# Kernel optimization log

Measured on AMD Instinct MI355X. Metric: run time of the kernel, lower is better.

## Reference

```python
import jax, jax.numpy as jnp
import numpy as np

NUM_HEADS = 64  # init kwarg


def _split_heads(x, num_heads):
    # torch: x.view(N, num_heads, head_size).permute(0, 2, 1) -> [N, head_size, num_heads]
    n, hidden = x.shape
    head_size = hidden // num_heads
    return x.reshape(n, num_heads, head_size).transpose(0, 2, 1)


def setup_inputs() -> dict:
    key = jax.random.key(0)
    kq, kk, kv = jax.random.split(key, 3)
    N, H = 4096, 4096
    q = jax.random.normal(kq, (N, H), dtype=jnp.float32)
    k = jax.random.normal(kk, (N, H), dtype=jnp.float32)
    v = jax.random.normal(kv, (N, H), dtype=jnp.float32)
    return {"q": q, "k": k, "v": v}


def reference(q, k, v):
    n, hidden = q.shape
    qh = _split_heads(q, NUM_HEADS)  # [N, d, h] with d=head_size, h=num_heads
    kh = _split_heads(k, NUM_HEADS)
    vh = _split_heads(v, NUM_HEADS)
    # scores: contraction over the num_heads axis (faithful to the original code)
    scores = jnp.einsum('ndh,neh->nde', qh, kh)      # [N, d, d]
    probs = jax.nn.softmax(scores, axis=-1)           # softmax over last dim, no scaling
    out = jnp.einsum('nde,neh->ndh', probs, vh)       # [N, d, h]
    # permute(0,2,1) then flatten -> [N, hidden]
    return out.transpose(0, 2, 1).reshape(n, hidden)
```

## Files before the change

kernel.cpp:

```cpp
#include <hip/hip_runtime.h>
#include <hip/hip_bf16.h>

typedef __bf16 bf16x8 __attribute__((ext_vector_type(8)));
typedef float  f32x4  __attribute__((ext_vector_type(4)));
typedef short  s16x8  __attribute__((ext_vector_type(8)));
typedef unsigned short u16;

static __device__ __forceinline__ u16 f2bf_rne(float f) {
  union { float f; unsigned u; } x; x.f = f;
  unsigned r = x.u + 0x7fffu + ((x.u >> 16) & 1u);
  return (u16)(r >> 16);
}

static __device__ __forceinline__ void splitbf(float f, short& hi, short& lo) {
  union { float f; unsigned u; } x; x.f = f;
  hi = (short)(x.u >> 16);
  union { unsigned u; float f; } h; h.u = x.u & 0xffff0000u;
  union { float f; unsigned u; } y; y.f = f - h.f;
  lo = (short)(y.u >> 16);
}

#define GLD_LDS16(g, l)                                                        \
  __builtin_amdgcn_global_load_lds(                                            \
      (const __attribute__((address_space(1))) void*)(g),                      \
      (__attribute__((address_space(3))) void*)(l), 16, 0, 0)

__global__ __launch_bounds__(256, 4)
void attn64_kernel(const float* __restrict__ q, const float* __restrict__ k,
                   const float* __restrict__ v, float* __restrict__ out)
{
  __shared__ float ldsQ[4096];
  __shared__ float ldsK[4096];

  const int tid  = threadIdx.x;
  const int wid  = tid >> 6;
  const int lane = tid & 63;
  const int quad = lane >> 4;
  const int lo   = lane & 15;
  const int row  = blockIdx.x;

  const float* qrow = q + (size_t)row * 4096;
  const float* krow = k + (size_t)row * 4096;
  const float* vrow = v + (size_t)row * 4096;
  float*       orow = out + (size_t)row * 4096;

  {
    const int hl = lane >> 4;
    const int e4 = (lane & 15) << 2;
#pragma unroll
    for (int i = 0; i < 8; ++i) {
      const int c   = wid * 8 + i;
      const int sec = c >> 4;
      const int c4  = c & 15;
      const int h   = c4 * 4 + hl;
      const int se  = e4 ^ (((h >> 3) & 1) << 4);
      const float* src = (sec ? krow : qrow) + h * 64 + se;
      GLD_LDS16(src, (sec ? ldsK : ldsQ) + c4 * 256);
    }
  }
  __syncthreads();

  f32x4 xv[8][2];
#pragma unroll
  for (int ks = 0; ks < 2; ++ks)
#pragma unroll
    for (int mt = 0; mt < 4; ++mt) {
      const float* p = vrow + (lo + 16 * mt) * 64 + quad * 8 + ks * 32;
      xv[ks * 4 + mt][0] = *(const f32x4*)p;
      xv[ks * 4 + mt][1] = *(const f32x4*)(p + 4);
    }
  __builtin_amdgcn_sched_barrier(0);

  s16x8 qh[2], ql[2];
  {
    const int dcol = wid * 16 + lo;
#pragma unroll
    for (int ks = 0; ks < 2; ++ks)
#pragma unroll
      for (int j = 0; j < 8; ++j) {
        const int h = ks * 32 + quad * 8 + j;
        float x = ldsQ[h * 64 + (dcol ^ ((quad & 1) << 4))];
        short hh, ll; splitbf(x, hh, ll);
        qh[ks][j] = hh; ql[ks][j] = ll;
      }
  }

  f32x4 acc[4];
#pragma unroll
  for (int et = 0; et < 4; ++et) acc[et] = (f32x4){0.f, 0.f, 0.f, 0.f};

#pragma unroll
  for (int et = 0; et < 4; ++et)
#pragma unroll
    for (int ks = 0; ks < 2; ++ks) {
      s16x8 kh, kl;
#pragma unroll
      for (int j = 0; j < 8; ++j) {
        const int h = ks * 32 + quad * 8 + j;
        float x = ldsK[h * 64 + ((lo + 16 * et) ^ ((quad & 1) << 4))];
        short hh, ll; splitbf(x, hh, ll);
        kh[j] = hh; kl[j] = ll;
      }
      bf16x8 ah = __builtin_bit_cast(bf16x8, qh[ks]);
      bf16x8 al = __builtin_bit_cast(bf16x8, ql[ks]);
      bf16x8 bh = __builtin_bit_cast(bf16x8, kh);
      bf16x8 bl = __builtin_bit_cast(bf16x8, kl);
      acc[et] = __builtin_amdgcn_mfma_f32_16x16x32_bf16(ah, bh, acc[et], 0, 0, 0);
      acc[et] = __builtin_amdgcn_mfma_f32_16x16x32_bf16(ah, bl, acc[et], 0, 0, 0);
      acc[et] = __builtin_amdgcn_mfma_f32_16x16x32_bf16(al, bh, acc[et], 0, 0, 0);
    }

#pragma unroll
  for (int r = 0; r < 4; ++r) {
    float m = fmaxf(fmaxf(acc[0][r], acc[1][r]), fmaxf(acc[2][r], acc[3][r]));
#pragma unroll
    for (int off = 1; off < 16; off <<= 1) m = fmaxf(m, __shfl_xor(m, off));
    float s = 0.f;
#pragma unroll
    for (int et = 0; et < 4; ++et) {
      float e0 = __expf(acc[et][r] - m);
      acc[et][r] = e0;
      s += e0;
    }
#pragma unroll
    for (int off = 1; off < 16; off <<= 1) s += __shfl_xor(s, off);
    float rs = 1.0f / s;
#pragma unroll
    for (int et = 0; et < 4; ++et) acc[et][r] *= rs;
  }

  __syncthreads();

  bf16x8 av[8];
#pragma unroll
  for (int i = 0; i < 8; ++i) {
    s16x8 tv;
#pragma unroll
    for (int j = 0; j < 4; ++j) {
      tv[j]     = (short)f2bf_rne(xv[i][0][j]);
      tv[4 + j] = (short)f2bf_rne(xv[i][1][j]);
    }
    av[i] = __builtin_bit_cast(bf16x8, tv);
  }

  float* P = ldsK;
#pragma unroll
  for (int r = 0; r < 4; ++r) {
    const int d   = wid * 16 + quad * 4 + r;
    const int swz = (d & 15) << 2;
#pragma unroll
    for (int et = 0; et < 4; ++et)
      P[d * 64 + ((lo + 16 * et) ^ swz)] = acc[et][r];
  }

  f32x4 acc2[4];
#pragma unroll
  for (int mt = 0; mt < 4; ++mt) acc2[mt] = (f32x4){0.f, 0.f, 0.f, 0.f};

#pragma unroll
  for (int ks = 0; ks < 2; ++ks) {
    const int eb    = quad * 8 + ks * 32;
    const int dmine = wid * 16 + lo;
    const int pswz  = lo << 2;
    f32x4 p0 = *(const f32x4*)&P[dmine * 64 + (eb ^ pswz)];
    f32x4 p1 = *(const f32x4*)&P[dmine * 64 + ((eb + 4) ^ pswz)];
    s16x8 tp;
#pragma unroll
    for (int j = 0; j < 4; ++j) {
      tp[j]     = (short)f2bf_rne(p0[j]);
      tp[4 + j] = (short)f2bf_rne(p1[j]);
    }
    bf16x8 bp = __builtin_bit_cast(bf16x8, tp);
#pragma unroll
    for (int mt = 0; mt < 4; ++mt)
      acc2[mt] = __builtin_amdgcn_mfma_f32_16x16x32_bf16(av[ks * 4 + mt], bp, acc2[mt], 0, 0, 0);
  }

#pragma unroll
  for (int mt = 0; mt < 4; ++mt)
#pragma unroll
    for (int r = 0; r < 4; ++r) {
      const int h = 16 * mt + quad * 4 + r;
      orow[h * 64 + wid * 16 + lo] = acc2[mt][r];
    }
}

extern "C" void kernel_launch(void* const* d_in, const int* in_sizes, int n_in,
                              void* d_out, int out_size, void* d_ws, size_t ws_size,
                              hipStream_t stream) {
  const float* q = (const float*)d_in[0];
  const float* k = (const float*)d_in[1];
  const float* v = (const float*)d_in[2];
  float* o = (float*)d_out;
  hipLaunchKernelGGL(attn64_kernel, dim3(4096), dim3(256), 0, stream, q, k, v, o);
}
```

Before: 215.6 us.

## Repartition second matmul so each wave owns an h-slice of V

The second GEMM (probs times V) is re-tiled so each wave owns 16 rows of h and loads only its own 2x8 V values, instead of every wave loading all of V and owning a d-slice. Each wave now reads all of P from LDS, so a barrier is added after the P stores. Global V traffic and register pressure per thread drop. In exchange, LDS reads of P rise fourfold and there is an extra synchronization point. Output stores become contiguous across nt-tiles within each h row.

```diff
diff --git a/kernel.cpp b/kernel.cpp
--- a/kernel.cpp
+++ b/kernel.cpp
@@ -60,15 +60,13 @@
   }
   __syncthreads();
 
-  f32x4 xv[8][2];
+  f32x4 xv[2][2];
 #pragma unroll
-  for (int ks = 0; ks < 2; ++ks)
-#pragma unroll
-    for (int mt = 0; mt < 4; ++mt) {
-      const float* p = vrow + (lo + 16 * mt) * 64 + quad * 8 + ks * 32;
-      xv[ks * 4 + mt][0] = *(const f32x4*)p;
-      xv[ks * 4 + mt][1] = *(const f32x4*)(p + 4);
-    }
+  for (int ks = 0; ks < 2; ++ks) {
+    const float* p = vrow + (wid * 16 + lo) * 64 + quad * 8 + ks * 32;
+    xv[ks][0] = *(const f32x4*)p;
+    xv[ks][1] = *(const f32x4*)(p + 4);
+  }
   __builtin_amdgcn_sched_barrier(0);
 
   s16x8 qh[2], ql[2];
@@ -131,18 +129,6 @@
 
   __syncthreads();
 
-  bf16x8 av[8];
-#pragma unroll
-  for (int i = 0; i < 8; ++i) {
-    s16x8 tv;
-#pragma unroll
-    for (int j = 0; j < 4; ++j) {
-      tv[j]     = (short)f2bf_rne(xv[i][0][j]);
-      tv[4 + j] = (short)f2bf_rne(xv[i][1][j]);
-    }
-    av[i] = __builtin_bit_cast(bf16x8, tv);
-  }
-
   float* P = ldsK;
 #pragma unroll
   for (int r = 0; r < 4; ++r) {
@@ -153,35 +139,50 @@
       P[d * 64 + ((lo + 16 * et) ^ swz)] = acc[et][r];
   }
 
+  __syncthreads();
+
+  bf16x8 av[2];
+#pragma unroll
+  for (int ks = 0; ks < 2; ++ks) {
+    s16x8 tv;
+#pragma unroll
+    for (int j = 0; j < 4; ++j) {
+      tv[j]     = (short)f2bf_rne(xv[ks][0][j]);
+      tv[4 + j] = (short)f2bf_rne(xv[ks][1][j]);
+    }
+    av[ks] = __builtin_bit_cast(bf16x8, tv);
+  }
+
   f32x4 acc2[4];
 #pragma unroll
-  for (int mt = 0; mt < 4; ++mt) acc2[mt] = (f32x4){0.f, 0.f, 0.f, 0.f};
+  for (int nt = 0; nt < 4; ++nt) acc2[nt] = (f32x4){0.f, 0.f, 0.f, 0.f};
 
 #pragma unroll
   for (int ks = 0; ks < 2; ++ks) {
-    const int eb    = quad * 8 + ks * 32;
-    const int dmine = wid * 16 + lo;
-    const int pswz  = lo << 2;
-    f32x4 p0 = *(const f32x4*)&P[dmine * 64 + (eb ^ pswz)];
-    f32x4 p1 = *(const f32x4*)&P[dmine * 64 + ((eb + 4) ^ pswz)];
-    s16x8 tp;
+    const int eb = quad * 8 + ks * 32;
 #pragma unroll
-    for (int j = 0; j < 4; ++j) {
-      tp[j]     = (short)f2bf_rne(p0[j]);
-      tp[4 + j] = (short)f2bf_rne(p1[j]);
+    for (int nt = 0; nt < 4; ++nt) {
+      const int d    = nt * 16 + lo;
+      const int pswz = lo << 2;
+      f32x4 p0 = *(const f32x4*)&P[d * 64 + (eb ^ pswz)];
+      f32x4 p1 = *(const f32x4*)&P[d * 64 + ((eb + 4) ^ pswz)];
+      s16x8 tp;
+#pragma unroll
+      for (int j = 0; j < 4; ++j) {
+        tp[j]     = (short)f2bf_rne(p0[j]);
+        tp[4 + j] = (short)f2bf_rne(p1[j]);
+      }
+      bf16x8 bp = __builtin_bit_cast(bf16x8, tp);
+      acc2[nt] = __builtin_amdgcn_mfma_f32_16x16x32_bf16(av[ks], bp, acc2[nt], 0, 0, 0);
     }
-    bf16x8 bp = __builtin_bit_cast(bf16x8, tp);
-#pragma unroll
-    for (int mt = 0; mt < 4; ++mt)
-      acc2[mt] = __builtin_amdgcn_mfma_f32_16x16x32_bf16(av[ks * 4 + mt], bp, acc2[mt], 0, 0, 0);
   }
 
 #pragma unroll
-  for (int mt = 0; mt < 4; ++mt)
+  for (int nt = 0; nt < 4; ++nt)
 #pragma unroll
     for (int r = 0; r < 4; ++r) {
-      const int h = 16 * mt + quad * 4 + r;
-      orow[h * 64 + wid * 16 + lo] = acc2[mt][r];
+      const int h = 16 * wid + quad * 4 + r;
+      orow[h * 64 + lo + 16 * nt] = acc2[nt][r];
     }
 }
 
```

Measured after the change: 214.5 us. About the same (-0.5%).
